# Kernel optimization log

Hardware: AMD Instinct MI355X
Metric: run time of the kernel (lower is better)

The kernel has to match this reference:

```python
import jax, jax.numpy as jnp
import numpy as np
from jax import lax

B = 65536

def _conv3(x, w, b):
    # x: [B,Cin,H,W], w: [Cout,Cin,3,3] (OIHW), SAME padding, stride 1
    y = lax.conv_general_dilated(x, w, (1, 1), 'SAME',
                                 dimension_numbers=('NCHW', 'OIHW', 'NCHW'))
    return y + b[None, :, None, None]

def _gru_cell(x, h, wu, bu, wr, br, wo, bo):
    s = jnp.concatenate([x, h], axis=1)
    update = jax.nn.sigmoid(_conv3(s, wu, bu))
    reset = jax.nn.sigmoid(_conv3(s, wr, br))
    out = jnp.tanh(_conv3(jnp.concatenate([x, h * reset], axis=1), wo, bo))
    return h * (1.0 - update) + out * update

def _mk_cell_params(key, cin, ch):
    ks = jax.random.split(key, 6)
    fan = (cin + ch) * 9
    sc = 1.0 / np.sqrt(fan)
    p = {}
    for i, g in enumerate(['u', 'r', 'o']):
        p['w' + g] = jax.random.normal(ks[2 * i], (ch, cin + ch, 3, 3), jnp.float32) * sc
        p['b' + g] = jax.random.normal(ks[2 * i + 1], (ch,), jnp.float32) * sc
    return p

def setup_inputs() -> dict:
    key = jax.random.key(0)
    k_in, k1, k2, k3, kd1, kd2 = jax.random.split(key, 6)
    inputs = jax.random.normal(k_in, (B, 1, 3, 3), jnp.float32)
    p1 = _mk_cell_params(k1, 1, 32)
    p2 = _mk_cell_params(k2, 32, 64)
    p3 = _mk_cell_params(k3, 64, 16)
    wd = jax.random.normal(kd1, (9, 16 * 3 * 3), jnp.float32) * (1.0 / 12.0)
    bd = jax.random.normal(kd2, (9,), jnp.float32) * (1.0 / 12.0)
    out = {'inputs': inputs, 'wd': wd, 'bd': bd}
    for i, p in enumerate([p1, p2, p3], start=1):
        for k, v in p.items():
            out[f'{k[0]}{i}{k[1]}'] = v  # e.g. w1u, b1u
    return out

def reference(inputs, wd, bd,
              w1u, b1u, w1r, b1r, w1o, b1o,
              w2u, b2u, w2r, b2r, w2o, b2o,
              w3u, b3u, w3r, b3r, w3o, b3o):
    b = inputs.shape[0]
    h1 = jnp.zeros((b, 32, 3, 3), inputs.dtype)
    h2 = jnp.zeros((b, 64, 3, 3), inputs.dtype)
    h3 = jnp.zeros((b, 16, 3, 3), inputs.dtype)
    x1 = _gru_cell(inputs, h1, w1u, b1u, w1r, b1r, w1o, b1o)
    x2 = _gru_cell(x1, h2, w2u, b2u, w2r, b2r, w2o, b2o)
    x3 = _gru_cell(x2, h3, w3u, b3u, w3r, b3r, w3o, b3o)
    out = x3.reshape(b, -1) @ wd.T + bd
    return (out, x1, x2, x3)
```

## Files before the change

kernel.cpp:

```cpp
#include <hip/hip_runtime.h>

#define BATCH 65536

typedef __attribute__((ext_vector_type(8))) short bf16x8;
typedef __attribute__((ext_vector_type(4))) float f32x4;

__device__ __forceinline__ unsigned short f2bf(float f) {
  unsigned int u = __float_as_uint(f);
  u += 0x7fffu + ((u >> 16) & 1u);
  return (unsigned short)(u >> 16);
}
__device__ __forceinline__ unsigned pack_trunc(float lo, float hi) {
  return __builtin_amdgcn_perm(__float_as_uint(hi), __float_as_uint(lo), 0x07060302u);
}

__device__ __forceinline__ float gru_act(float u, float o) {
  u = fmaxf(u, -60.0f);
  o = fmaxf(o, -30.0f);
  float a  = __expf(-u);
  float a2 = __expf(-2.0f * o);
  return (1.0f - a2) * __builtin_amdgcn_rcpf((1.0f + a) * (1.0f + a2));
}

__device__ __forceinline__ float conv_tap(const float* __restrict__ w, int co, int ci,
                                          int p, int q, int CINTOT) {
  int pi = p / 3, pj = p % 3, qi = q / 3, qj = q % 3;
  int di = qi - pi + 1, dj = qj - pj + 1;
  if ((unsigned)di < 3u && (unsigned)dj < 3u)
    return w[((co * CINTOT + ci) * 3 + di) * 3 + dj];
  return 0.0f;
}

__global__ void build_bt2f(const float* __restrict__ wu, const float* __restrict__ wo,
                           unsigned short* __restrict__ BTF) {
  int e = blockIdx.x * 256 + threadIdx.x;
  if (e >= 331776) return;
  int g = e / 165888;
  int rem = e - g * 165888;
  int n = rem / 288, k = rem - n * 288;
  int cf = n >> 4, lr = n & 15, kt = k >> 5, jc = (k >> 3) & 3, s = k & 7;
  unsigned dst = ((((unsigned)(g * 36 + cf) * 9 + kt) * 64 + jc * 16 + lr) * 8 + s);
  BTF[dst] = f2bf(conv_tap(g ? wo : wu, n / 9, k / 9, n % 9, k % 9, 96));
}
__global__ void build_bt3f(const float* __restrict__ wu, const float* __restrict__ wo,
                           unsigned short* __restrict__ BTF) {
  int e = blockIdx.x * 256 + threadIdx.x;
  if (e >= 165888) return;
  int g = e / 82944;
  int rem = e - g * 82944;
  int n = rem / 576, k = rem - n * 576;
  int cf = n >> 4, lr = n & 15, kt = k >> 5, jc = (k >> 3) & 3, s = k & 7;
  unsigned dst = ((((unsigned)(g * 9 + cf) * 18 + kt) * 64 + jc * 16 + lr) * 8 + s);
  BTF[dst] = f2bf(conv_tap(g ? wo : wu, n / 9, k / 9, n % 9, k % 9, 80));
}
__global__ void build_bt1f(const float* __restrict__ wu, const float* __restrict__ wo,
                           unsigned short* __restrict__ BTF) {
  int e = blockIdx.x * 256 + threadIdx.x;
  if (e >= 18432) return;
  int g = e / 9216;
  int rem = e - g * 9216;
  int n = rem / 32, k = rem - n * 32;
  int cf = n >> 4, lr = n & 15, jc = (k >> 3) & 3, s = k & 7;
  unsigned dst = (((unsigned)(g * 18 + cf) * 64 + jc * 16 + lr) * 8 + s);
  float v = (k < 9) ? conv_tap(g ? wo : wu, n / 9, 0, n % 9, k, 33) : 0.0f;
  BTF[dst] = f2bf(v);
}

#define OFF_X1L 0
#define OFF_X3L 0
#define OFF_WL 20480
#define OFF_BLB 25664
#define OFF_XL2 40960
#define OFF_AL 40960
#define SMEM_BYTES 50176

#define L1_CHUNK(BREG, CH) do {                                              \
    f32x4 acc1[4][2][3] = {};                                                \
    _Pragma("unroll") for (int m_ = 0; m_ < 4; ++m_)                         \
      _Pragma("unroll") for (int g_ = 0; g_ < 2; ++g_)                       \
        _Pragma("unroll") for (int f_ = 0; f_ < 3; ++f_)                     \
          acc1[m_][g_][f_] = __builtin_amdgcn_mfma_f32_16x16x32_bf16(        \
              afx[m_], BREG[g_][f_], acc1[m_][g_][f_], 0, 0, 0);             \
    _Pragma("unroll") for (int m_ = 0; m_ < 4; ++m_)                         \
      _Pragma("unroll") for (int f_ = 0; f_ < 3; ++f_) {                     \
        int n_ = (CH) * 144 + (wid * 3 + f_) * 16 + lrow;                    \
        float bU_ = b1u[n_ / 9], bO_ = b1o[n_ / 9];                          \
        f32x4 uv_ = acc1[m_][0][f_], ov_ = acc1[m_][1][f_];                  \
        _Pragma("unroll") for (int t_ = 0; t_ < 4; ++t_) {                   \
          int r_ = m_ * 16 + jc * 4 + t_;                                    \
          float v_ = gru_act(uv_[t_] + bU_, ov_[t_] + bO_);                  \
          x1[(size_t)(r0 + r_) * 288 + n_] = v_;                             \
          *(unsigned short*)(x1l + r_ * 640 + (((n_ >> 3) ^ (r_ & 7)) << 4) + (n_ & 7) * 2) = \
              (unsigned short)(__float_as_uint(v_) >> 16);                   \
        }                                                                    \
      }                                                                      \
  } while (0)

#define L2_STEP(CUR, NXT, LAST) do {                                         \
    if (!(LAST)) {                                                           \
      _Pragma("unroll") for (int g_ = 0; g_ < 2; ++g_)                       \
        _Pragma("unroll") for (int f_ = 0; f_ < 3; ++f_)                     \
          NXT[g_][f_] = *(const bf16x8*)(BT2b + ldoff + offB2[g_][f_]);      \
      if (ktn == 8) { ktn = 0; ldoff += 102400u; }                           \
      else { ++ktn; ldoff += 1024u; }                                        \
    }                                                                        \
    bf16x8 af_[4];                                                           \
    const int c8_ = kt * 4 + jc;                                             \
    _Pragma("unroll") for (int m_ = 0; m_ < 4; ++m_)                         \
      af_[m_] = *(const bf16x8*)(aBase[m_] + ((c8_ ^ aXor[m_]) << 4));       \
    _Pragma("unroll") for (int m_ = 0; m_ < 4; ++m_)                         \
      _Pragma("unroll") for (int g_ = 0; g_ < 2; ++g_)                       \
        _Pragma("unroll") for (int f_ = 0; f_ < 3; ++f_)                     \
          acc[m_][g_][f_] = __builtin_amdgcn_mfma_f32_16x16x32_bf16(         \
              af_[m_], CUR[g_][f_], acc[m_][g_][f_], 0, 0, 0);               \
    if (kt == 8) {                                                           \
      _Pragma("unroll") for (int m_ = 0; m_ < 4; ++m_)                       \
        _Pragma("unroll") for (int f_ = 0; f_ < 3; ++f_) {                   \
          int n_ = n0 + (wid * 3 + f_) * 16 + lrow;                          \
          float bU_ = b2u[n_ / 9], bO_ = b2o[n_ / 9];                        \
          f32x4 uv_ = acc[m_][0][f_], ov_ = acc[m_][1][f_];                  \
          _Pragma("unroll") for (int t_ = 0; t_ < 4; ++t_) {                 \
            int r_ = r0 + m_ * 16 + jc * 4 + t_;                             \
            x2[(size_t)r_ * 576 + n_] = gru_act(uv_[t_] + bU_, ov_[t_] + bO_); \
          }                                                                  \
          acc[m_][0][f_] = (f32x4){0.f, 0.f, 0.f, 0.f};                      \
          acc[m_][1][f_] = (f32x4){0.f, 0.f, 0.f, 0.f};                      \
        }                                                                    \
      kt = 0; n0 += 192;                                                     \
    } else ++kt;                                                             \
  } while (0)

#define L3_STEP(CURB, NXTB) do {                                             \
    {                                                                        \
      uint4 h_;                                                              \
      h_.x = pack_trunc(pa0.x, pa0.y);                                       \
      h_.y = pack_trunc(pa0.z, pa0.w);                                       \
      h_.z = pack_trunc(pa1.x, pa1.y);                                       \
      h_.w = pack_trunc(pa1.z, pa1.w);                                       \
      *(uint4*)wAl = h_;                                                     \
    }                                                                        \
    __syncthreads();                  \
    if (kt3 < 17) {                                                          \
      const float* gp_ = pA + (kt3 + 1) * 32;                                \
      pa0 = *(const float4*)gp_;                                             \
      pa1 = *(const float4*)(gp_ + 4);                                       \
      if (wid < 3) {                                                         \
        _Pragma("unroll") for (int g_ = 0; g_ < 2; ++g_)                     \
          _Pragma("unroll") for (int f_ = 0; f_ < 3; ++f_)                   \
            NXTB[g_][f_] = *(const bf16x8*)(BT3b + b3ld + offB3[g_][f_]);    \
      }                                                                      \
      b3ld += 1024u;                                                         \
    }                                                                        \
    if (wid < 3) {                                                           \
      bf16x8 af_[4];                                                         \
      _Pragma("unroll") for (int m_ = 0; m_ < 4; ++m_)                       \
        af_[m_] = *(const bf16x8*)(rA3[m_]);                                 \
      _Pragma("unroll") for (int m_ = 0; m_ < 4; ++m_)                       \
        _Pragma("unroll") for (int g_ = 0; g_ < 2; ++g_)                     \
          _Pragma("unroll") for (int f_ = 0; f_ < 3; ++f_)                   \
            acc[m_][g_][f_] = __builtin_amdgcn_mfma_f32_16x16x32_bf16(       \
                af_[m_], CURB[g_][f_], acc[m_][g_][f_], 0, 0, 0);            \
    }                                                                        \
    __syncthreads();                                                         \
    ++kt3;                                                                   \
  } while (0)

__global__ __launch_bounds__(256, 2) void megafused(
    const float* __restrict__ xin, const unsigned short* __restrict__ BT1F,
    const float* __restrict__ b1u, const float* __restrict__ b1o,
    const unsigned short* __restrict__ BT2F,
    const float* __restrict__ b2u, const float* __restrict__ b2o,
    const unsigned short* __restrict__ BT3F,
    const float* __restrict__ b3u, const float* __restrict__ b3o,
    const float* __restrict__ wd, const float* __restrict__ bd,
    float* __restrict__ x1, float* __restrict__ x2,
    float* __restrict__ x3, float* __restrict__ out) {
  __shared__ __align__(16) char smem[SMEM_BYTES];
  char* x1l = smem + OFF_X1L;
  char* Al = smem + OFF_AL;
  unsigned short* x3l = (unsigned short*)(smem + OFF_X3L);
  float* xl2 = (float*)(smem + OFF_XL2);
  float* wl = (float*)(smem + OFF_WL);
  float* blb = (float*)(smem + OFF_BLB);

  const int tid = threadIdx.x;
  const int lane = tid & 63;
  const int wid = tid >> 6;
  const int lrow = lane & 15;
  const int jc = lane >> 4;
  const int r0 = blockIdx.x * 64;

  const char* BT1b = (const char*)BT1F;
  const char* BT2b = (const char*)BT2F;
  const char* BT3b = (const char*)BT3F;
  const unsigned laneB = (unsigned)lane * 16u;

  unsigned offB1[2][3], offB2[2][3], offB3[2][3];
#pragma unroll
  for (int g = 0; g < 2; ++g)
#pragma unroll
    for (int f = 0; f < 3; ++f) {
      offB1[g][f] = (unsigned)(g * 18 + wid * 3 + f) * 1024u + laneB;
      offB2[g][f] = (unsigned)(g * 36 + wid * 3 + f) * 9216u + laneB;
      offB3[g][f] = (unsigned)(g * 9 + wid * 3 + f) * 18432u + laneB;
    }

  bf16x8 b1a[2][3], b1b[2][3], bX[2][3], bY[2][3];
  if (wid < 3) {
#pragma unroll
    for (int g = 0; g < 2; ++g)
#pragma unroll
      for (int f = 0; f < 3; ++f) {
        b1a[g][f] = *(const bf16x8*)(BT1b + offB1[g][f]);
        b1b[g][f] = *(const bf16x8*)(BT1b + 9216u + offB1[g][f]);
      }
  }
#pragma unroll
  for (int g = 0; g < 2; ++g)
#pragma unroll
    for (int f = 0; f < 3; ++f)
      bX[g][f] = *(const bf16x8*)(BT2b + offB2[g][f]);

  for (int c = tid; c < 2304; c += 256) {
    int row = c / 36, col = c - row * 36;
    xl2[c] = (col < 9) ? xin[(size_t)(r0 + row) * 9 + col] : 0.0f;
  }
  __syncthreads();

  bf16x8 afx[4];
#pragma unroll
  for (int m = 0; m < 4; ++m) {
    const float* xr = xl2 + (m * 16 + lrow) * 36 + jc * 8;
    float4 a0 = *(const float4*)xr;
    float4 a1 = *(const float4*)(xr + 4);
    union { uint4 u; bf16x8 v; } cv;
    cv.u.x = pack_trunc(a0.x, a0.y);
    cv.u.y = pack_trunc(a0.z, a0.w);
    cv.u.z = pack_trunc(a1.x, a1.y);
    cv.u.w = pack_trunc(a1.z, a1.w);
    afx[m] = cv.v;
  }

  if (wid < 3) {
    L1_CHUNK(b1a, 0);
    L1_CHUNK(b1b, 1);
  }
  __syncthreads();

  {
    const char* aBase[4];
    int aXor[4];
#pragma unroll
    for (int m = 0; m < 4; ++m) {
      int row = m * 16 + lrow;
      aBase[m] = x1l + row * 640;
      aXor[m] = row & 7;
    }
    f32x4 acc[4][2][3] = {};
    int kt = 0, n0 = 0, ktn = 1;
    unsigned ldoff = 1024u;
    for (int sp = 0; sp < 13; ++sp) {
      L2_STEP(bX, bY, false);
      L2_STEP(bY, bX, false);
    }
    L2_STEP(bX, bY, true);
  }
  __syncthreads();

  for (int c = tid; c < 1296; c += 256) wl[c] = wd[c];
  if (tid < 9) blb[tid] = bd[tid];

  {
    const float* pA = x2 + (size_t)(r0 + (tid >> 2)) * 576 + (tid & 3) * 8;
    char* wAl = Al + (tid >> 2) * 64 + (((tid & 3) ^ (((tid >> 2) >> 1) & 3)) << 4);
    float4 pa0 = *(const float4*)pA;
    float4 pa1 = *(const float4*)(pA + 4);
    bf16x8 b3a[2][3], b3b[2][3];
    if (wid < 3) {
#pragma unroll
      for (int g = 0; g < 2; ++g)
#pragma unroll
        for (int f = 0; f < 3; ++f)
          b3a[g][f] = *(const bf16x8*)(BT3b + offB3[g][f]);
    }
    const char* rA3[4];
#pragma unroll
    for (int m = 0; m < 4; ++m) {
      int row = m * 16 + lrow;
      rA3[m] = Al + row * 64 + ((jc ^ ((row >> 1) & 3)) << 4);
    }

    f32x4 acc[4][2][3] = {};
    int kt3 = 0;
    unsigned b3ld = 1024u;
    for (int kp = 0; kp < 9; ++kp) {
      L3_STEP(b3a, b3b);
      L3_STEP(b3b, b3a);
    }
    if (wid < 3) {
#pragma unroll
      for (int m = 0; m < 4; ++m)
#pragma unroll
        for (int f = 0; f < 3; ++f) {
          int n = (wid * 3 + f) * 16 + lrow;
          float bU = b3u[n / 9], bO = b3o[n / 9];
          f32x4 uv = acc[m][0][f], ov = acc[m][1][f];
#pragma unroll
          for (int t = 0; t < 4; ++t) {
            int r = m * 16 + jc * 4 + t;
            float v = gru_act(uv[t] + bU, ov[t] + bO);
            x3[(size_t)(r0 + r) * 144 + n] = v;
            x3l[r * 146 + n] = (unsigned short)(__float_as_uint(v) >> 16);
          }
        }
    }
  }
  __syncthreads();

  if (wid < 3) {
    int drow = lane;
    int jb = wid * 3;
    float s0 = blb[jb], s1 = blb[jb + 1], s2 = blb[jb + 2];
    for (int k = 0; k < 144; k += 2) {
      unsigned pr = *(const unsigned*)&x3l[drow * 146 + k];
      float v0 = __uint_as_float(pr << 16);
      float v1 = __uint_as_float(pr & 0xffff0000u);
      const float2 w0 = *(const float2*)&wl[jb * 144 + k];
      const float2 w1 = *(const float2*)&wl[(jb + 1) * 144 + k];
      const float2 w2 = *(const float2*)&wl[(jb + 2) * 144 + k];
      s0 = fmaf(v0, w0.x, s0); s0 = fmaf(v1, w0.y, s0);
      s1 = fmaf(v0, w1.x, s1); s1 = fmaf(v1, w1.y, s1);
      s2 = fmaf(v0, w2.x, s2); s2 = fmaf(v1, w2.y, s2);
    }
    size_t ob = (size_t)(r0 + drow) * 9 + jb;
    out[ob] = s0; out[ob + 1] = s1; out[ob + 2] = s2;
  }
}

extern "C" void kernel_launch(void* const* d_in, const int* in_sizes, int n_in,
                              void* d_out, int out_size, void* d_ws, size_t ws_size,
                              hipStream_t stream) {
  const float* inputs = (const float*)d_in[0];
  const float* wd  = (const float*)d_in[1];
  const float* bd  = (const float*)d_in[2];
  const float* w1u = (const float*)d_in[3];
  const float* b1u = (const float*)d_in[4];
  const float* w1o = (const float*)d_in[7];
  const float* b1o = (const float*)d_in[8];
  const float* w2u = (const float*)d_in[9];
  const float* b2u = (const float*)d_in[10];
  const float* w2o = (const float*)d_in[13];
  const float* b2o = (const float*)d_in[14];
  const float* w3u = (const float*)d_in[15];
  const float* b3u = (const float*)d_in[16];
  const float* w3o = (const float*)d_in[19];
  const float* b3o = (const float*)d_in[20];

  float* out = (float*)d_out;
  float* x1 = out + (size_t)BATCH * 9;
  float* x2 = x1 + (size_t)BATCH * 288;
  float* x3 = x2 + (size_t)BATCH * 576;

  unsigned short* BT2F = (unsigned short*)d_ws;
  unsigned short* BT3F = BT2F + 331776;
  unsigned short* BT1F = BT3F + 165888;

  build_bt2f<<<1296, 256, 0, stream>>>(w2u, w2o, BT2F);
  build_bt3f<<<648, 256, 0, stream>>>(w3u, w3o, BT3F);
  build_bt1f<<<72, 256, 0, stream>>>(w1u, w1o, BT1F);

  megafused<<<BATCH / 64, 256, 0, stream>>>(inputs, BT1F, b1u, b1o, BT2F, b2u, b2o,
                                            BT3F, b3u, b3o, wd, bd, x1, x2, x3, out);
}
```

Measured before the change: 145.4 us.

## Use persistent blocks with atomic tile scheduler and direct-register layer-3 A operands

Launches a fixed grid of 768 persistent blocks that pull 64-row tiles from a global atomic counter instead of one block per tile. Layer 3 now loads x2 rows directly into registers per wave and converts them to bf16 MFMA operands, removing the LDS staging buffer and the two barriers per k-step. Occupancy hint is raised to 3 blocks per SM. The trade-offs are extra atomic traffic, an extra init kernel, redundant per-wave global loads of x2, and possible register pressure from the higher occupancy target.

```diff
diff --git a/kernel.cpp b/kernel.cpp
--- a/kernel.cpp
+++ b/kernel.cpp
@@ -1,6 +1,7 @@
 #include <hip/hip_runtime.h>
 
 #define BATCH 65536
+#define NTILES 1024
 
 typedef __attribute__((ext_vector_type(8))) short bf16x8;
 typedef __attribute__((ext_vector_type(4))) float f32x4;
@@ -66,12 +67,13 @@
   BTF[dst] = f2bf(v);
 }
 
+__global__ void init_counter(unsigned* __restrict__ c) { *c = 0u; }
+
 #define OFF_X1L 0
 #define OFF_X3L 0
 #define OFF_WL 20480
 #define OFF_BLB 25664
 #define OFF_XL2 40960
-#define OFF_AL 40960
 #define SMEM_BYTES 50176
 
 #define L1_CHUNK(BREG, CH) do {                                              \
@@ -130,42 +132,35 @@
     } else ++kt;                                                             \
   } while (0)
 
-#define L3_STEP(CURB, NXTB) do {                                             \
-    {                                                                        \
-      uint4 h_;                                                              \
-      h_.x = pack_trunc(pa0.x, pa0.y);                                       \
-      h_.y = pack_trunc(pa0.z, pa0.w);                                       \
-      h_.z = pack_trunc(pa1.x, pa1.y);                                       \
-      h_.w = pack_trunc(pa1.z, pa1.w);                                       \
-      *(uint4*)wAl = h_;                                                     \
+#define L3_STEP(CURB, NXTB, LAST) do {                                       \
+    bf16x8 af_[4];                                                           \
+    _Pragma("unroll") for (int m_ = 0; m_ < 4; ++m_) {                       \
+      union { uint4 u; bf16x8 v; } cv_;                                      \
+      cv_.u.x = pack_trunc(pa0[m_].x, pa0[m_].y);                            \
+      cv_.u.y = pack_trunc(pa0[m_].z, pa0[m_].w);                            \
+      cv_.u.z = pack_trunc(pa1[m_].x, pa1[m_].y);                            \
+      cv_.u.w = pack_trunc(pa1[m_].z, pa1[m_].w);                            \
+      af_[m_] = cv_.v;                                                       \
     }                                                                        \
-    __syncthreads();                  \
-    if (kt3 < 17) {                                                          \
-      const float* gp_ = pA + (kt3 + 1) * 32;                                \
-      pa0 = *(const float4*)gp_;                                             \
-      pa1 = *(const float4*)(gp_ + 4);                                       \
-      if (wid < 3) {                                                         \
-        _Pragma("unroll") for (int g_ = 0; g_ < 2; ++g_)                     \
-          _Pragma("unroll") for (int f_ = 0; f_ < 3; ++f_)                   \
-            NXTB[g_][f_] = *(const bf16x8*)(BT3b + b3ld + offB3[g_][f_]);    \
+    if (!(LAST)) {                                                           \
+      _Pragma("unroll") for (int m_ = 0; m_ < 4; ++m_) {                     \
+        pa0[m_] = *(const float4*)(x2r[m_] + a3off);                         \
+        pa1[m_] = *(const float4*)(x2r[m_] + a3off + 4);                     \
       }                                                                      \
+      a3off += 32;                                                           \
+      _Pragma("unroll") for (int g_ = 0; g_ < 2; ++g_)                       \
+        _Pragma("unroll") for (int f_ = 0; f_ < 3; ++f_)                     \
+          NXTB[g_][f_] = *(const bf16x8*)(BT3b + b3ld + offB3[g_][f_]);      \
       b3ld += 1024u;                                                         \
     }                                                                        \
-    if (wid < 3) {                                                           \
-      bf16x8 af_[4];                                                         \
-      _Pragma("unroll") for (int m_ = 0; m_ < 4; ++m_)                       \
-        af_[m_] = *(const bf16x8*)(rA3[m_]);                                 \
-      _Pragma("unroll") for (int m_ = 0; m_ < 4; ++m_)                       \
-        _Pragma("unroll") for (int g_ = 0; g_ < 2; ++g_)                     \
-          _Pragma("unroll") for (int f_ = 0; f_ < 3; ++f_)                   \
-            acc[m_][g_][f_] = __builtin_amdgcn_mfma_f32_16x16x32_bf16(       \
-                af_[m_], CURB[g_][f_], acc[m_][g_][f_], 0, 0, 0);            \
-    }                                                                        \
-    __syncthreads();                                                         \
-    ++kt3;                                                                   \
+    _Pragma("unroll") for (int m_ = 0; m_ < 4; ++m_)                         \
+      _Pragma("unroll") for (int g_ = 0; g_ < 2; ++g_)                       \
+        _Pragma("unroll") for (int f_ = 0; f_ < 3; ++f_)                     \
+          acc[m_][g_][f_] = __builtin_amdgcn_mfma_f32_16x16x32_bf16(         \
+              af_[m_], CURB[g_][f_], acc[m_][g_][f_], 0, 0, 0);              \
   } while (0)
 
-__global__ __launch_bounds__(256, 2) void megafused(
+__global__ __launch_bounds__(256, 3) void megafused(
     const float* __restrict__ xin, const unsigned short* __restrict__ BT1F,
     const float* __restrict__ b1u, const float* __restrict__ b1o,
     const unsigned short* __restrict__ BT2F,
@@ -173,11 +168,12 @@
     const unsigned short* __restrict__ BT3F,
     const float* __restrict__ b3u, const float* __restrict__ b3o,
     const float* __restrict__ wd, const float* __restrict__ bd,
+    unsigned* __restrict__ tctr,
     float* __restrict__ x1, float* __restrict__ x2,
     float* __restrict__ x3, float* __restrict__ out) {
   __shared__ __align__(16) char smem[SMEM_BYTES];
+  __shared__ int tile_s;
   char* x1l = smem + OFF_X1L;
-  char* Al = smem + OFF_AL;
   unsigned short* x3l = (unsigned short*)(smem + OFF_X3L);
   float* xl2 = (float*)(smem + OFF_XL2);
   float* wl = (float*)(smem + OFF_WL);
@@ -188,7 +184,6 @@
   const int wid = tid >> 6;
   const int lrow = lane & 15;
   const int jc = lane >> 4;
-  const int r0 = blockIdx.x * 64;
 
   const char* BT1b = (const char*)BT1F;
   const char* BT2b = (const char*)BT2F;
@@ -204,100 +199,108 @@
       offB2[g][f] = (unsigned)(g * 36 + wid * 3 + f) * 9216u + laneB;
       offB3[g][f] = (unsigned)(g * 9 + wid * 3 + f) * 18432u + laneB;
     }
-
-  bf16x8 b1a[2][3], b1b[2][3], bX[2][3], bY[2][3];
-  if (wid < 3) {
+  const char* aBase[4];
+  int aXor[4];
+#pragma unroll
+  for (int m = 0; m < 4; ++m) {
+    int row = m * 16 + lrow;
+    aBase[m] = x1l + row * 640;
+    aXor[m] = row & 7;
+  }
+
+  for (;;) {
+    if (tid == 0) tile_s = (int)atomicAdd(tctr, 1u);
+    __syncthreads();
+    const int tile = tile_s;
+    if (tile >= NTILES) break;
+    const int r0 = tile * 64;
+
+    bf16x8 b1a[2][3], b1b[2][3], bX[2][3], bY[2][3];
+    if (wid < 3) {
+#pragma unroll
+      for (int g = 0; g < 2; ++g)
+#pragma unroll
+        for (int f = 0; f < 3; ++f) {
+          b1a[g][f] = *(const bf16x8*)(BT1b + offB1[g][f]);
+          b1b[g][f] = *(const bf16x8*)(BT1b + 9216u + offB1[g][f]);
+        }
+    }
 #pragma unroll
     for (int g = 0; g < 2; ++g)
 #pragma unroll
-      for (int f = 0; f < 3; ++f) {
-        b1a[g][f] = *(const bf16x8*)(BT1b + offB1[g][f]);
-        b1b[g][f] = *(const bf16x8*)(BT1b + 9216u + offB1[g][f]);
+      for (int f = 0; f < 3; ++f)
+        bX[g][f] = *(const bf16x8*)(BT2b + offB2[g][f]);
+
+    for (int c = tid; c < 2304; c += 256) {
+      int row = c / 36, col = c - row * 36;
+      xl2[c] = (col < 9) ? xin[(size_t)(r0 + row) * 9 + col] : 0.0f;
+    }
+    __syncthreads();
+
+    bf16x8 afx[4];
+#pragma unroll
+    for (int m = 0; m < 4; ++m) {
+      const float* xr = xl2 + (m * 16 + lrow) * 36 + jc * 8;
+      float4 a0 = *(const float4*)xr;
+      float4 a1 = *(const float4*)(xr + 4);
+      union { uint4 u; bf16x8 v; } cv;
+      cv.u.x = pack_trunc(a0.x, a0.y);
+      cv.u.y = pack_trunc(a0.z, a0.w);
+      cv.u.z = pack_trunc(a1.x, a1.y);
+      cv.u.w = pack_trunc(a1.z, a1.w);
+      afx[m] = cv.v;
+    }
+
+    if (wid < 3) {
+      L1_CHUNK(b1a, 0);
+      L1_CHUNK(b1b, 1);
+    }
+    __syncthreads();
+
+    {
+      f32x4 acc[4][2][3] = {};
+      int kt = 0, n0 = 0, ktn = 1;
+      unsigned ldoff = 1024u;
+      for (int sp = 0; sp < 13; ++sp) {
+        L2_STEP(bX, bY, false);
+        L2_STEP(bY, bX, false);
       }
-  }
-#pragma unroll
-  for (int g = 0; g < 2; ++g)
-#pragma unroll
-    for (int f = 0; f < 3; ++f)
-      bX[g][f] = *(const bf16x8*)(BT2b + offB2[g][f]);
-
-  for (int c = tid; c < 2304; c += 256) {
-    int row = c / 36, col = c - row * 36;
-    xl2[c] = (col < 9) ? xin[(size_t)(r0 + row) * 9 + col] : 0.0f;
-  }
-  __syncthreads();
-
-  bf16x8 afx[4];
-#pragma unroll
-  for (int m = 0; m < 4; ++m) {
-    const float* xr = xl2 + (m * 16 + lrow) * 36 + jc * 8;
-    float4 a0 = *(const float4*)xr;
-    float4 a1 = *(const float4*)(xr + 4);
-    union { uint4 u; bf16x8 v; } cv;
-    cv.u.x = pack_trunc(a0.x, a0.y);
-    cv.u.y = pack_trunc(a0.z, a0.w);
-    cv.u.z = pack_trunc(a1.x, a1.y);
-    cv.u.w = pack_trunc(a1.z, a1.w);
-    afx[m] = cv.v;
-  }
-
-  if (wid < 3) {
-    L1_CHUNK(b1a, 0);
-    L1_CHUNK(b1b, 1);
-  }
-  __syncthreads();
-
-  {
-    const char* aBase[4];
-    int aXor[4];
-#pragma unroll
-    for (int m = 0; m < 4; ++m) {
-      int row = m * 16 + lrow;
-      aBase[m] = x1l + row * 640;
-      aXor[m] = row & 7;
-    }
-    f32x4 acc[4][2][3] = {};
-    int kt = 0, n0 = 0, ktn = 1;
-    unsigned ldoff = 1024u;
-    for (int sp = 0; sp < 13; ++sp) {
-      L2_STEP(bX, bY, false);
-      L2_STEP(bY, bX, false);
-    }
-    L2_STEP(bX, bY, true);
-  }
-  __syncthreads();
-
-  for (int c = tid; c < 1296; c += 256) wl[c] = wd[c];
-  if (tid < 9) blb[tid] = bd[tid];
-
-  {
-    const float* pA = x2 + (size_t)(r0 + (tid >> 2)) * 576 + (tid & 3) * 8;
-    char* wAl = Al + (tid >> 2) * 64 + (((tid & 3) ^ (((tid >> 2) >> 1) & 3)) << 4);
-    float4 pa0 = *(const float4*)pA;
-    float4 pa1 = *(const float4*)(pA + 4);
-    bf16x8 b3a[2][3], b3b[2][3];
+      L2_STEP(bX, bY, true);
+    }
+    __syncthreads();
+
+    for (int c = tid; c < 1296; c += 256) wl[c] = wd[c];
+    if (tid < 9) blb[tid] = bd[tid];
+
     if (wid < 3) {
+      const float* x2r[4];
+#pragma unroll
+      for (int m = 0; m < 4; ++m)
+        x2r[m] = x2 + (size_t)(r0 + m * 16 + lrow) * 576 + jc * 8;
+
+      float4 pa0[4], pa1[4];
+#pragma unroll
+      for (int m = 0; m < 4; ++m) {
+        pa0[m] = *(const float4*)(x2r[m]);
+        pa1[m] = *(const float4*)(x2r[m] + 4);
+      }
+      bf16x8 b3a[2][3], b3b[2][3];
 #pragma unroll
       for (int g = 0; g < 2; ++g)
 #pragma unroll
         for (int f = 0; f < 3; ++f)
           b3a[g][f] = *(const bf16x8*)(BT3b + offB3[g][f]);
-    }
-    const char* rA3[4];
-#pragma unroll
-    for (int m = 0; m < 4; ++m) {
-      int row = m * 16 + lrow;
-      rA3[m] = Al + row * 64 + ((jc ^ ((row >> 1) & 3)) << 4);
-    }
-
-    f32x4 acc[4][2][3] = {};
-    int kt3 = 0;
-    unsigned b3ld = 1024u;
-    for (int kp = 0; kp < 9; ++kp) {
-      L3_STEP(b3a, b3b);
-      L3_STEP(b3b, b3a);
-    }
-    if (wid < 3) {
+
+      f32x4 acc[4][2][3] = {};
+      int a3off = 32;
+      unsigned b3ld = 1024u;
+      for (int kp = 0; kp < 8; ++kp) {
+        L3_STEP(b3a, b3b, false);
+        L3_STEP(b3b, b3a, false);
+      }
+      L3_STEP(b3a, b3b, false);
+      L3_STEP(b3b, b3a, true);
+
 #pragma unroll
       for (int m = 0; m < 4; ++m)
 #pragma unroll
@@ -314,26 +317,26 @@
           }
         }
     }
-  }
-  __syncthreads();
-
-  if (wid < 3) {
-    int drow = lane;
-    int jb = wid * 3;
-    float s0 = blb[jb], s1 = blb[jb + 1], s2 = blb[jb + 2];
-    for (int k = 0; k < 144; k += 2) {
-      unsigned pr = *(const unsigned*)&x3l[drow * 146 + k];
-      float v0 = __uint_as_float(pr << 16);
-      float v1 = __uint_as_float(pr & 0xffff0000u);
-      const float2 w0 = *(const float2*)&wl[jb * 144 + k];
-      const float2 w1 = *(const float2*)&wl[(jb + 1) * 144 + k];
-      const float2 w2 = *(const float2*)&wl[(jb + 2) * 144 + k];
-      s0 = fmaf(v0, w0.x, s0); s0 = fmaf(v1, w0.y, s0);
-      s1 = fmaf(v0, w1.x, s1); s1 = fmaf(v1, w1.y, s1);
-      s2 = fmaf(v0, w2.x, s2); s2 = fmaf(v1, w2.y, s2);
-    }
-    size_t ob = (size_t)(r0 + drow) * 9 + jb;
-    out[ob] = s0; out[ob + 1] = s1; out[ob + 2] = s2;
+    __syncthreads();
+
+    if (wid < 3) {
+      int drow = lane;
+      int jb = wid * 3;
+      float s0 = blb[jb], s1 = blb[jb + 1], s2 = blb[jb + 2];
+      for (int k = 0; k < 144; k += 2) {
+        unsigned pr = *(const unsigned*)&x3l[drow * 146 + k];
+        float v0 = __uint_as_float(pr << 16);
+        float v1 = __uint_as_float(pr & 0xffff0000u);
+        const float2 w0 = *(const float2*)&wl[jb * 144 + k];
+        const float2 w1 = *(const float2*)&wl[(jb + 1) * 144 + k];
+        const float2 w2 = *(const float2*)&wl[(jb + 2) * 144 + k];
+        s0 = fmaf(v0, w0.x, s0); s0 = fmaf(v1, w0.y, s0);
+        s1 = fmaf(v0, w1.x, s1); s1 = fmaf(v1, w1.y, s1);
+        s2 = fmaf(v0, w2.x, s2); s2 = fmaf(v1, w2.y, s2);
+      }
+      size_t ob = (size_t)(r0 + drow) * 9 + jb;
+      out[ob] = s0; out[ob + 1] = s1; out[ob + 2] = s2;
+    }
   }
 }
 
@@ -364,11 +367,13 @@
   unsigned short* BT2F = (unsigned short*)d_ws;
   unsigned short* BT3F = BT2F + 331776;
   unsigned short* BT1F = BT3F + 165888;
+  unsigned* tctr = (unsigned*)(BT1F + 18432);
 
   build_bt2f<<<1296, 256, 0, stream>>>(w2u, w2o, BT2F);
   build_bt3f<<<648, 256, 0, stream>>>(w3u, w3o, BT3F);
   build_bt1f<<<72, 256, 0, stream>>>(w1u, w1o, BT1F);
-
-  megafused<<<BATCH / 64, 256, 0, stream>>>(inputs, BT1F, b1u, b1o, BT2F, b2u, b2o,
-                                            BT3F, b3u, b3o, wd, bd, x1, x2, x3, out);
-}
+  init_counter<<<1, 1, 0, stream>>>(tctr);
+
+  megafused<<<768, 256, 0, stream>>>(inputs, BT1F, b1u, b1o, BT2F, b2u, b2o,
+                                     BT3F, b3u, b3o, wd, bd, tctr, x1, x2, x3, out);
+}
```

Measured after the change: 559.9 us. +285.1%, slower.
